# Performance work log

Hardware: AMD Instinct MI355X
Metric: run time of the kernel (lower is better)

The kernel has to match this reference:

```python
import jax, jax.numpy as jnp
import numpy as np
from jax import lax

B, C, O, K, H, W = 8, 16, 16, 3, 512, 512
STRIDE, PAD = 1, 1
BN_EPS = 1e-5


def setup_inputs() -> dict:
    key = jax.random.key(0)
    ks = jax.random.split(key, 5)
    # kaiming_normal fan_out for a (O, I, K, K, K) tensor: fan_out = O * K**3
    std = float(np.sqrt(2.0 / (O * K ** 3)))
    return {
        "x": jax.random.normal(ks[0], (B, C, H, W), jnp.float32),
        "w_fft_real": jax.random.normal(ks[1], (O, C, K, K, K), jnp.float32) * std,
        "w_fft_imag": jax.random.normal(ks[2], (O, C, K, K, K), jnp.float32) * std,
        "rot_w": jax.random.normal(ks[3], (3, C), jnp.float32) * float(np.sqrt(1.0 / C)),
        "rot_b": jnp.zeros((3,), jnp.float32),
        "bn_gamma": jnp.ones((3,), jnp.float32),
        "bn_beta": jnp.zeros((3,), jnp.float32),
    }


def _forward(x, w_fft_real, w_fft_imag, rot_w, rot_b, bn_gamma, bn_beta):
    # --- rotation params: 1x1 conv -> BatchNorm2d (training-mode batch stats) ---
    z = jnp.einsum("bchw,oc->bohw", x, rot_w) + rot_b[None, :, None, None]  # (B,3,H,W)
    mu = jnp.mean(z, axis=(0, 2, 3), keepdims=True)
    var = jnp.mean((z - mu) ** 2, axis=(0, 2, 3), keepdims=True)  # biased, as torch BN
    z = (z - mu) * lax.rsqrt(var + BN_EPS)
    z = z * bn_gamma[None, :, None, None] + bn_beta[None, :, None, None]
    angles = jnp.mean(z, axis=(2, 3))            # (B,3)
    angle = jnp.sum(angles, axis=1, keepdims=True)  # (B,1)
    angle = jnp.tanh(angle) * (jnp.pi / 4)
    cos_theta = jnp.cos(angle)[:, 0]             # (B,)

    # --- FFT-domain phase rotation of the 3D kernel ---
    freq = jnp.fft.fftfreq(K).astype(jnp.float32)
    fx, fy, fz = jnp.meshgrid(freq, freq, freq, indexing="ij")
    fsum = fx + fy + fz                           # (K,K,K)
    phase = jnp.exp(-2j * jnp.pi * (cos_theta[:, None, None, None] * fsum))  # (B,K,K,K) complex
    w_fft = (w_fft_real + 1j * w_fft_imag)        # (O,C,K,K,K)
    w_rot = w_fft[None] * phase[:, None, None]    # (B,O,C,K,K,K)
    rotated = jnp.fft.ifftn(w_rot, axes=(-3, -2, -1)).real

    # --- take middle depth slice -> per-sample 2D kernels ---
    mid = K // 2
    w2d = rotated[:, :, :, mid, :, :]             # (B,O,C,K,K)
    gw = w2d.reshape(B * O, C, K, K)

    # --- batch-as-groups conv2d ---
    xg = x.reshape(1, B * C, H, W)
    out = lax.conv_general_dilated(
        xg, gw,
        window_strides=(STRIDE, STRIDE),
        padding=[(PAD, PAD), (PAD, PAD)],
        feature_group_count=B,
        dimension_numbers=("NCHW", "OIHW", "NCHW"),
    )
    return out.reshape(B, O, out.shape[2], out.shape[3])


def reference(x, w_fft_real, w_fft_imag, rot_w, rot_b, bn_gamma, bn_beta):
    return _forward(x, w_fft_real, w_fft_imag, rot_w, rot_b, bn_gamma, bn_beta)
```

## Files before the change

### kernel.cpp

```cpp
#include <hip/hip_runtime.h>

#define HW 262144
#define CIN 16
#define OUTC 16

#define WS_PARTIALS 0
#define WS_COS      12288
#define WS_WB_F     12296

typedef float  floatx4 __attribute__((ext_vector_type(4)));
typedef short  bf16x8  __attribute__((ext_vector_type(8)));

__device__ __forceinline__ ushort bf16_rne(float f) {
  unsigned u = __float_as_uint(f);
  unsigned r = (u + 0x7FFFu + ((u >> 16) & 1u)) >> 16;
  return (ushort)r;
}
__device__ __forceinline__ void bf16_split(float f, ushort& hi, ushort& lo) {
  hi = bf16_rne(f);
  float fh = __uint_as_float(((unsigned)hi) << 16);
  lo = bf16_rne(f - fh);
}

__global__ __launch_bounds__(256) void k_reduce(const float* __restrict__ x,
                                                const float* __restrict__ rot_w,
                                                const float* __restrict__ rot_b,
                                                float* __restrict__ partials) {
  const int blk = blockIdx.x;
  const int b = blk >> 8;
  const int s = blk & 255;
  const int t = threadIdx.x;

  float rw[3][16];
#pragma unroll
  for (int k = 0; k < 3; k++)
#pragma unroll
    for (int c = 0; c < 16; c++) rw[k][c] = rot_w[k * 16 + c];
  float rb[3];
#pragma unroll
  for (int k = 0; k < 3; k++) rb[k] = rot_b[k];

  const float* xb = x + (size_t)b * CIN * HW + s * 1024 + t * 4;

  float z[3][4];
#pragma unroll
  for (int k = 0; k < 3; k++)
#pragma unroll
    for (int j = 0; j < 4; j++) z[k][j] = 0.f;

#pragma unroll
  for (int c = 0; c < 16; c++) {
    float4 v = *reinterpret_cast<const float4*>(xb + (size_t)c * HW);
#pragma unroll
    for (int k = 0; k < 3; k++) {
      z[k][0] += rw[k][c] * v.x;
      z[k][1] += rw[k][c] * v.y;
      z[k][2] += rw[k][c] * v.z;
      z[k][3] += rw[k][c] * v.w;
    }
  }

  float vals[6];
#pragma unroll
  for (int k = 0; k < 3; k++) {
    float sz = 0.f, sz2 = 0.f;
#pragma unroll
    for (int j = 0; j < 4; j++) {
      float zz = z[k][j] + rb[k];
      sz += zz;
      sz2 += zz * zz;
    }
    vals[k] = sz;
    vals[3 + k] = sz2;
  }

  __shared__ float redsh[4][6];
  const int wave = t >> 6, lane = t & 63;
#pragma unroll
  for (int v = 0; v < 6; v++) {
    float val = vals[v];
#pragma unroll
    for (int off = 32; off; off >>= 1) val += __shfl_down(val, off, 64);
    if (lane == 0) redsh[wave][v] = val;
  }
  __syncthreads();
  if (t < 6)
    partials[blk * 6 + t] = redsh[0][t] + redsh[1][t] + redsh[2][t] + redsh[3][t];
}

__global__ __launch_bounds__(256) void k_stats(const float* __restrict__ partials,
                                               const float* __restrict__ bn_gamma,
                                               const float* __restrict__ bn_beta,
                                               float* __restrict__ cos_theta) {
  __shared__ float Msh[8][3];
  __shared__ float varsum[3];
  const int t = threadIdx.x;

  if (t < 24) {
    int b = t / 3, c = t - b * 3;
    float s = 0.f;
    for (int i = 0; i < 256; i++) s += partials[(b * 256 + i) * 6 + c];
    Msh[b][c] = s;
  }
  if (t >= 64) {
    int c = (t - 64) >> 6;
    int lane = t & 63;
    float s = 0.f;
    for (int i = lane; i < 2048; i += 64) s += partials[i * 6 + 3 + c];
#pragma unroll
    for (int off = 32; off; off >>= 1) s += __shfl_down(s, off, 64);
    if (lane == 0) varsum[c] = s;
  }
  __syncthreads();

  if (t < 8) {
    const float invN = 1.0f / (8.0f * 262144.0f);
    const float invHW = 1.0f / 262144.0f;
    float angle = 0.f;
#pragma unroll
    for (int c = 0; c < 3; c++) {
      float tot = 0.f;
#pragma unroll
      for (int b = 0; b < 8; b++) tot += Msh[b][c];
      float mu = tot * invN;
      float var = varsum[c] * invN - mu * mu;
      float rs = rsqrtf(var + 1e-5f);
      angle += (Msh[t][c] * invHW - mu) * rs * bn_gamma[c] + bn_beta[c];
    }
    float a = tanhf(angle) * 0.7853981633974483f;
    cos_theta[t] = cosf(a);
  }
}

__global__ __launch_bounds__(256) void k_rotw(const float* __restrict__ wfr,
                                              const float* __restrict__ wfi,
                                              const float* __restrict__ cos_theta,
                                              ushort* __restrict__ wB) {
  const int b = blockIdx.x;
  const int t = threadIdx.x;
  const int o = t & 15;
  const int c = t >> 4;

  const float ct = cos_theta[b];
  const float phi = ct * 2.0943951023931953f;
  float sp, cp;
  sincosf(phi, &sp, &cp);
  const float ur[3] = {1.f, cp, cp};
  const float ui[3] = {0.f, -sp, sp};
  const float wr3[3] = {1.f, -0.5f, -0.5f};
  const float wi3[3] = {0.f, 0.8660254037844386f, -0.8660254037844386f};

  float cr[3][3], ci[3][3];
#pragma unroll
  for (int k = 0; k < 3; k++)
#pragma unroll
    for (int m = 0; m < 3; m++) {
      int e = (k * m) % 3;
      cr[k][m] = ur[k] * wr3[e] - ui[k] * wi3[e];
      ci[k][m] = ur[k] * wi3[e] + ui[k] * wr3[e];
    }

  const float* Ar = wfr + (o * 16 + c) * 27;
  const float* Ai = wfi + (o * 16 + c) * 27;

  float outv[9];
#pragma unroll
  for (int i = 0; i < 9; i++) outv[i] = 0.f;

#pragma unroll
  for (int k1 = 0; k1 < 3; k1++) {
    float ar[9], ai[9];
#pragma unroll
    for (int i = 0; i < 9; i++) { ar[i] = Ar[k1 * 9 + i]; ai[i] = Ai[k1 * 9 + i]; }
    float hr[3][3], hi2[3][3];
#pragma unroll
    for (int k2 = 0; k2 < 3; k2++)
#pragma unroll
      for (int q = 0; q < 3; q++) {
        float sr = 0.f, si = 0.f;
#pragma unroll
        for (int k3 = 0; k3 < 3; k3++) {
          float xr = ar[k2 * 3 + k3], xi = ai[k2 * 3 + k3];
          sr += xr * cr[k3][q] - xi * ci[k3][q];
          si += xr * ci[k3][q] + xi * cr[k3][q];
        }
        hr[k2][q] = sr;
        hi2[k2][q] = si;
      }
    float drr = cr[k1][1], dii = ci[k1][1];
#pragma unroll
    for (int p = 0; p < 3; p++)
#pragma unroll
      for (int q = 0; q < 3; q++) {
        float sr = 0.f, si = 0.f;
#pragma unroll
        for (int k2 = 0; k2 < 3; k2++) {
          sr += hr[k2][q] * cr[k2][p] - hi2[k2][q] * ci[k2][p];
          si += hr[k2][q] * ci[k2][p] + hi2[k2][q] * cr[k2][p];
        }
        outv[p * 3 + q] += sr * drr - si * dii;
      }
  }

#pragma unroll
  for (int tap = 0; tap < 9; tap++) {
    float v = outv[tap] * (1.0f / 27.0f);
    int k = tap * 16 + c;
    int kb = k >> 5;
    int g = (k >> 3) & 3;
    int j = k & 7;
    int ln = g * 16 + o;
    ushort hi, lo;
    bf16_split(v, hi, lo);
    int idx = ((b * 5 + kb) * 2) * 512 + ln * 8 + j;
    wB[idx] = hi;
    wB[idx + 512] = lo;
  }

#pragma unroll
  for (int u = 0; u < 2; u++) {
    int e = t * 2 + u;
    int hl = e >> 8;
    int rem = e & 255;
    int kk = 144 + (rem >> 4);
    int o2 = rem & 15;
    int g2 = (kk >> 3) & 3;
    int ln2 = g2 * 16 + o2;
    int j2 = kk & 7;
    wB[((b * 5 + 4) * 2 + hl) * 512 + ln2 * 8 + j2] = 0;
  }
}

__global__ __launch_bounds__(256, 4) void k_conv(const float* __restrict__ x,
                                                 const ushort* __restrict__ wB,
                                                 float* __restrict__ out) {
  __shared__ ushort xsb[18 * 1096];

  const int b = blockIdx.z;
  const int col0 = blockIdx.x * 32;
  const int row0 = blockIdx.y * 16;
  const int t = threadIdx.x;
  const int lane = t & 63;

  const ushort* wBb = wB + b * 5120;
  bf16x8 wh[5], wl[5];
#pragma unroll
  for (int kb = 0; kb < 5; kb++) {
    wh[kb] = *reinterpret_cast<const bf16x8*>(wBb + (kb * 2 + 0) * 512 + lane * 8);
    wl[kb] = *reinterpret_cast<const bf16x8*>(wBb + (kb * 2 + 1) * 512 + lane * 8);
  }

  const float* xb = x + (size_t)b * CIN * HW;
  for (int i = t; i < 2304; i += 256) {
    int c = i / 144;
    int rem = i - c * 144;
    int r = rem >> 3;
    int grp = rem & 7;
    int gr = row0 - 1 + r;
    int gc = col0 + grp * 4;
    float4 v = make_float4(0.f, 0.f, 0.f, 0.f);
    if ((unsigned)gr < 512u)
      v = *reinterpret_cast<const float4*>(xb + (size_t)c * HW + gr * 512 + gc);
    float vv[4] = {v.x, v.y, v.z, v.w};
    int colb = grp * 4 + 1;
#pragma unroll
    for (int j = 0; j < 4; j++) {
      ushort hi, lo;
      bf16_split(vv[j], hi, lo);
      int col = colb + j;
      int base = r * 1096 + col * 32;
      int swz = (col >> 1) & 3;
      int ch = (c >> 3) ^ swz;
      xsb[base + ch * 8 + (c & 7)] = hi;
      xsb[base + (ch ^ 2) * 8 + (c & 7)] = lo;
    }
  }
  for (int i = t; i < 576; i += 256) {
    int c = i / 36;
    int rem = i - c * 36;
    int r = rem >> 1;
    int side = rem & 1;
    int col = side ? 33 : 0;
    int gr = row0 - 1 + r;
    int gc = col0 - 1 + side * 33;
    float v = 0.f;
    if ((unsigned)gr < 512u && (unsigned)gc < 512u)
      v = xb[(size_t)c * HW + gr * 512 + gc];
    ushort hi, lo;
    bf16_split(v, hi, lo);
    int base = r * 1096 + col * 32;
    int swz = (col >> 1) & 3;
    int ch = (c >> 3) ^ swz;
    xsb[base + ch * 8 + (c & 7)] = hi;
    xsb[base + (ch ^ 2) * 8 + (c & 7)] = lo;
  }

  const int m = lane & 15;
  const int g = lane >> 4;
  const int chalf = g & 1;
  const int tsel = g >> 1;
  int offh[5], offl[5];
#pragma unroll
  for (int kb = 0; kb < 5; kb++) {
    int tap = kb * 2 + tsel;
    if (tap > 8) tap = 8;
    int dy = tap / 3;
    int dx = tap - dy * 3;
    int mdx = m + dx;
    int swz = (mdx >> 1) & 3;
    offh[kb] = dy * 1096 + mdx * 32 + ((chalf ^ swz) << 3);
    offl[kb] = dy * 1096 + mdx * 32 + (((2 | chalf) ^ swz) << 3);
  }

  __syncthreads();

  const int w = t >> 6;
  const int oo = lane & 15;
  const int quad = lane >> 4;
#pragma unroll
  for (int s = 0; s < 8; s++) {
    int r = w * 4 + (s >> 1);
    int cg = s & 1;
    int base = r * 1096 + cg * 512;
    floatx4 acc = {0.f, 0.f, 0.f, 0.f};
#pragma unroll
    for (int kb = 0; kb < 5; kb++) {
      bf16x8 a_hi = *reinterpret_cast<const bf16x8*>(&xsb[base + offh[kb]]);
      bf16x8 a_lo = *reinterpret_cast<const bf16x8*>(&xsb[base + offl[kb]]);
      acc = __builtin_amdgcn_mfma_f32_16x16x32_bf16(a_hi, wh[kb], acc, 0, 0, 0);
      acc = __builtin_amdgcn_mfma_f32_16x16x32_bf16(a_hi, wl[kb], acc, 0, 0, 0);
      acc = __builtin_amdgcn_mfma_f32_16x16x32_bf16(a_lo, wh[kb], acc, 0, 0, 0);
    }
    float* dst = out + (size_t)(b * OUTC + oo) * HW + (size_t)(row0 + r) * 512 +
                 col0 + cg * 16 + quad * 4;
    *reinterpret_cast<float4*>(dst) = make_float4(acc[0], acc[1], acc[2], acc[3]);
  }
}

extern "C" void kernel_launch(void* const* d_in, const int* in_sizes, int n_in,
                              void* d_out, int out_size, void* d_ws, size_t ws_size,
                              hipStream_t stream) {
  const float* x      = (const float*)d_in[0];
  const float* wfr    = (const float*)d_in[1];
  const float* wfi    = (const float*)d_in[2];
  const float* rot_w  = (const float*)d_in[3];
  const float* rot_b  = (const float*)d_in[4];
  const float* bn_g   = (const float*)d_in[5];
  const float* bn_b   = (const float*)d_in[6];
  float* out = (float*)d_out;
  float* ws  = (float*)d_ws;

  float* partials = ws + WS_PARTIALS;
  float* cosw     = ws + WS_COS;
  ushort* wB      = (ushort*)(ws + WS_WB_F);

  k_reduce<<<2048, 256, 0, stream>>>(x, rot_w, rot_b, partials);
  k_stats<<<1, 256, 0, stream>>>(partials, bn_g, bn_b, cosw);
  k_rotw<<<8, 256, 0, stream>>>(wfr, wfi, cosw, wB);
  dim3 grid(16, 32, 8);
  k_conv<<<grid, 256, 0, stream>>>(x, wB, out);
}
```

Measured before the change: 318.2 us.

## Remap conv blocks across XCDs and stage halo tile with vectorized LDS stores

```diff
diff --git a/kernel.cpp b/kernel.cpp
--- a/kernel.cpp
+++ b/kernel.cpp
@@ -236,9 +236,12 @@
                                                  float* __restrict__ out) {
   __shared__ ushort xsb[18 * 1096];
 
-  const int b = blockIdx.z;
-  const int col0 = blockIdx.x * 32;
-  const int row0 = blockIdx.y * 16;
+  const int id = blockIdx.x;
+  const int nid = (id & 7) * 512 + (id >> 3);
+  const int b = nid >> 9;
+  const int rem0 = nid & 511;
+  const int row0 = (rem0 >> 4) * 16;
+  const int col0 = (rem0 & 15) * 32;
   const int t = threadIdx.x;
   const int lane = t & 63;
 
@@ -251,48 +254,32 @@
   }
 
   const float* xb = x + (size_t)b * CIN * HW;
-  for (int i = t; i < 2304; i += 256) {
-    int c = i / 144;
-    int rem = i - c * 144;
-    int r = rem >> 3;
-    int grp = rem & 7;
-    int gr = row0 - 1 + r;
-    int gc = col0 + grp * 4;
-    float4 v = make_float4(0.f, 0.f, 0.f, 0.f);
-    if ((unsigned)gr < 512u)
-      v = *reinterpret_cast<const float4*>(xb + (size_t)c * HW + gr * 512 + gc);
-    float vv[4] = {v.x, v.y, v.z, v.w};
-    int colb = grp * 4 + 1;
-#pragma unroll
-    for (int j = 0; j < 4; j++) {
-      ushort hi, lo;
-      bf16_split(vv[j], hi, lo);
-      int col = colb + j;
-      int base = r * 1096 + col * 32;
+#pragma unroll
+  for (int it = 0; it < 5; it++) {
+    int p = it * 256 + t;
+    if (p < 1224) {
+      int row = p / 68;
+      int rem2 = p - row * 68;
+      int col = rem2 >> 1;
+      int chalf = rem2 & 1;
+      int gr = row0 - 1 + row;
+      int gc = col0 - 1 + col;
+      bool ok = ((unsigned)gr < 512u) && ((unsigned)gc < 512u);
+      const float* src = xb + (size_t)(chalf * 8) * HW + gr * 512 + gc;
+      bf16x8 hv, lv;
+#pragma unroll
+      for (int j = 0; j < 8; j++) {
+        float v = ok ? src[(size_t)j * HW] : 0.f;
+        ushort hi, lo;
+        bf16_split(v, hi, lo);
+        hv[j] = (short)hi;
+        lv[j] = (short)lo;
+      }
       int swz = (col >> 1) & 3;
-      int ch = (c >> 3) ^ swz;
-      xsb[base + ch * 8 + (c & 7)] = hi;
-      xsb[base + (ch ^ 2) * 8 + (c & 7)] = lo;
-    }
-  }
-  for (int i = t; i < 576; i += 256) {
-    int c = i / 36;
-    int rem = i - c * 36;
-    int r = rem >> 1;
-    int side = rem & 1;
-    int col = side ? 33 : 0;
-    int gr = row0 - 1 + r;
-    int gc = col0 - 1 + side * 33;
-    float v = 0.f;
-    if ((unsigned)gr < 512u && (unsigned)gc < 512u)
-      v = xb[(size_t)c * HW + gr * 512 + gc];
-    ushort hi, lo;
-    bf16_split(v, hi, lo);
-    int base = r * 1096 + col * 32;
-    int swz = (col >> 1) & 3;
-    int ch = (c >> 3) ^ swz;
-    xsb[base + ch * 8 + (c & 7)] = hi;
-    xsb[base + (ch ^ 2) * 8 + (c & 7)] = lo;
+      int base = row * 1096 + col * 32;
+      *reinterpret_cast<bf16x8*>(&xsb[base + ((chalf ^ swz) << 3)]) = hv;
+      *reinterpret_cast<bf16x8*>(&xsb[base + (((2 | chalf) ^ swz) << 3)]) = lv;
+    }
   }
 
   const int m = lane & 15;
@@ -357,6 +344,5 @@
   k_reduce<<<2048, 256, 0, stream>>>(x, rot_w, rot_b, partials);
   k_stats<<<1, 256, 0, stream>>>(partials, bn_g, bn_b, cosw);
   k_rotw<<<8, 256, 0, stream>>>(wfr, wfi, cosw, wB);
-  dim3 grid(16, 32, 8);
-  k_conv<<<grid, 256, 0, stream>>>(x, wB, out);
-}
+  k_conv<<<4096, 256, 0, stream>>>(x, wB, out);
+}
```

Result: faster. 296.2 us (-6.9%).
